# Optimization experiments

Hardware: AMD Instinct MI355X
Metric: run time of the kernel (lower is better)

The kernel has to match this reference:

```python
import jax, jax.numpy as jnp
import numpy as np

# ---- LIF moment-mapping constants (MNN defaults: V_th=20, V_res=0, L=0.05, T_ref=5) ----
L_COND = 0.05
SQRT_L = float(np.sqrt(L_COND))
V_TH, V_RES, T_REF = 20.0, 0.0, 5.0
CLIP = 4.0            # clamp integration bounds to keep exp(x^2) in fp32 range
BN_EPS = 1e-5
SQRT_PI_HALF = float(np.sqrt(np.pi) / 2.0)

_nodes, _weights = np.polynomial.legendre.leggauss(16)
NODES = jnp.asarray(_nodes, jnp.float32)     # [Q]
WEIGHTS = jnp.asarray(_weights, jnp.float32)  # [Q]


def _g(x):
    # Dawson-like integrand: e^{x^2} * sqrt(pi)/2 * (1 + erf(x))
    return jnp.exp(x * x) * (SQRT_PI_HALF * (1.0 + jax.lax.erf(x)))


def _q(t):
    # integrand of the second-order (variance) Dawson function
    e = SQRT_PI_HALF * (1.0 + jax.lax.erf(t))
    return jnp.exp(t * t) * e * e


def _moment_activation(u, s, rho):
    """Mnn_Activate_Mean / Std / Corr: LIF moment mapping via fixed Gauss-Legendre quadrature."""
    s_safe = jnp.maximum(s, 1e-6)
    ub = jnp.clip((V_TH * L_COND - u) / (s_safe * SQRT_L), -CLIP, CLIP)
    lb = jnp.clip((V_RES * L_COND - u) / (s_safe * SQRT_L), -CLIP, CLIP)
    mid, half = 0.5 * (ub + lb), 0.5 * (ub - lb)
    x = mid[..., None] + half[..., None] * NODES            # [B,N,Q]
    I1 = half * jnp.sum(WEIGHTS * _g(x), axis=-1)           # int_{lb}^{ub} g
    u_a = 1.0 / (T_REF + (2.0 / L_COND) * I1)               # mean firing rate
    # variance of ISI: (8/L^2) int_{lb}^{ub} e^{x^2} h(x) dx, h(x)= int_{-CLIP}^{x} q(t) dt
    hm = 0.5 * (x + CLIP)                                   # inner half-width, [B,N,Q]
    t = 0.5 * (x - CLIP)[..., None] + hm[..., None] * NODES  # [B,N,Q,Q]
    h = hm * jnp.sum(WEIGHTS * _q(t), axis=-1)              # [B,N,Q]
    V = half * jnp.sum(WEIGHTS * jnp.exp(x * x) * h, axis=-1)
    var_T = (8.0 / (L_COND * L_COND)) * V
    s_a = jnp.sqrt(jnp.maximum(u_a ** 3 * var_T, 0.0))      # std of firing rate
    # linear-response susceptibility for correlation propagation
    chi = u_a * u_a * (2.0 / L_COND) * (_g(ub) - _g(lb)) / (SQRT_L * jnp.maximum(s_a, 1e-6))
    rho_a = rho * chi[:, :, None] * chi[:, None, :]
    n = rho.shape[-1]
    idx = jnp.arange(n)
    rho_a = rho_a.at[:, idx, idx].set(1.0)
    return u_a, s_a, rho_a


def setup_inputs() -> dict:
    key = jax.random.key(0)
    k = jax.random.split(key, 6)
    B, NIN, NOUT = 512, 256, 256
    u = jax.random.normal(k[0], (B, NIN), jnp.float32) + 1.0
    s = jax.random.uniform(k[1], (B, NIN), jnp.float32, minval=0.1, maxval=1.5)
    # valid correlation matrix: normalized low-rank Gram matrix
    A = jax.random.normal(k[2], (B, NIN, 64), jnp.float32)
    cov = jnp.einsum('bik,bjk->bij', A, A) / 64.0
    d = jnp.sqrt(jnp.diagonal(cov, axis1=1, axis2=2))
    rho = cov / (d[:, :, None] * d[:, None, :] + 1e-6)
    W = jax.random.normal(k[3], (NOUT, NIN), jnp.float32) / np.sqrt(NIN)
    b = jax.random.normal(k[4], (NOUT,), jnp.float32) * 0.01
    gamma = jnp.full((NOUT,), 2.5, jnp.float32)  # bn_mean.weight filled with 2.5
    beta = jnp.full((NOUT,), 2.5, jnp.float32)   # bn_mean.bias filled with 2.5
    return {"u": u, "s": s, "rho": rho, "W": W, "b": b, "gamma": gamma, "beta": beta}


def reference(u, s, rho, W, b, gamma, beta):
    # Mnn_Linear_Corr: propagate (mean, std, corr) through a linear map
    u2 = u @ W.T + b                                        # [B,NOUT]
    cov = rho * s[:, :, None] * s[:, None, :]               # input covariance
    cov = jnp.einsum('oi,bij->boj', W, cov)
    cov = jnp.einsum('boj,pj->bop', cov, W)                 # W C W^T
    var_diag = jnp.diagonal(cov, axis1=1, axis2=2)
    s2 = jnp.sqrt(jnp.maximum(var_diag, 0.0))
    rho2 = cov / (s2[:, :, None] * s2[:, None, :] + 1e-12)
    # BatchNorm1d on mean (training stats) + consistent std scaling (Mnn_Std_Bn1d, bias=False)
    mu = jnp.mean(u2, axis=0)
    var = jnp.mean((u2 - mu) ** 2, axis=0)
    inv = gamma / jnp.sqrt(var + BN_EPS)
    s_bn = s2 * jnp.abs(inv)
    u_bn = (u2 - mu) * inv + beta
    return _moment_activation(u_bn, s_bn, rho2)
```

## Files before the change

kernel.cpp:

```cpp
#include <hip/hip_runtime.h>
#include <math.h>

#define NB 512
#define NN 256

typedef __bf16 bf16x8 __attribute__((ext_vector_type(8)));
typedef float f32x16 __attribute__((ext_vector_type(16)));

constexpr float C_ERF   = 0.88622692545275801f;
constexpr float SQRT_PI = 1.77245385090551603f;
constexpr float SQRTL   = 0.22360679774997896f;

__device__ __constant__ float GLN[16] = {
  -0.98940093499164993f, -0.94457502307323258f, -0.86563120238783174f,
  -0.75540440835500303f, -0.61787624440264375f, -0.45801677765722739f,
  -0.28160355077925891f, -0.09501250983763744f,  0.09501250983763744f,
   0.28160355077925891f,  0.45801677765722739f,  0.61787624440264375f,
   0.75540440835500303f,  0.86563120238783174f,  0.94457502307323258f,
   0.98940093499164993f };
__device__ __constant__ float GLW[16] = {
   0.02715245941175409f, 0.06225352393864789f, 0.09515851168249278f,
   0.12462897125553387f, 0.14959598881657673f, 0.16915651939500254f,
   0.18260341504492358f, 0.18945061045506850f, 0.18945061045506850f,
   0.18260341504492358f, 0.16915651939500254f, 0.14959598881657673f,
   0.12462897125553387f, 0.09515851168249278f, 0.06225352393864789f,
   0.02715245941175409f };

__device__ __forceinline__ float fast_P(float z) {
  float r = __builtin_amdgcn_rcpf(fmaf(0.5f, z, 1.0f));
  float p = fmaf(r, 0.17087277f, -0.82215223f);
  p = fmaf(r, p, 1.48851587f);
  p = fmaf(r, p, -1.13520398f);
  p = fmaf(r, p, 0.27886807f);
  p = fmaf(r, p, -0.18628806f);
  p = fmaf(r, p, 0.09678418f);
  p = fmaf(r, p, 0.37409196f);
  p = fmaf(r, p, 1.00002368f);
  p = fmaf(r, p, -1.26551223f);
  return C_ERF * r * __expf(p);
}
__device__ __forceinline__ float fast_EE(float x, float E) {
  float P = fast_P(fabsf(x));
  return x <= 0.0f ? P : fmaf(SQRT_PI, E, -P);
}

__device__ __forceinline__ uint bfrn(float x) {
  uint u = __float_as_uint(x);
  return (u + 0x7fffu + ((u >> 16) & 1u)) >> 16;
}
__device__ __forceinline__ uint packhi(float a, float b) {
  return bfrn(a) | (bfrn(b) << 16);
}
__device__ __forceinline__ uint packlo(float a, float b, uint h) {
  float af = __uint_as_float(h << 16);
  float bf = __uint_as_float(h & 0xffff0000u);
  return bfrn(a - af) | (bfrn(b - bf) << 16);
}
__device__ __forceinline__ void stage8(ushort* hiP, ushort* loP, int row, int halfk,
                                       float4 f0, float4 f1) {
  uint h0 = packhi(f0.x, f0.y), h1 = packhi(f0.z, f0.w);
  uint h2 = packhi(f1.x, f1.y), h3 = packhi(f1.z, f1.w);
  uint l0 = packlo(f0.x, f0.y, h0), l1 = packlo(f0.z, f0.w, h1);
  uint l2 = packlo(f1.x, f1.y, h2), l3 = packlo(f1.z, f1.w, h3);
  int lane = halfk * 32 + (row & 31);
  int base = ((row >> 5) * 64 + lane) * 8;
  *(uint4*)&hiP[base] = make_uint4(h0, h1, h2, h3);
  *(uint4*)&loP[base] = make_uint4(l0, l1, l2, l3);
}

__global__ __launch_bounds__(256) void k_u2(const float* __restrict__ u,
                                            const float* __restrict__ W,
                                            const float* __restrict__ bias,
                                            float* __restrict__ u2) {
  int b = blockIdx.x, t = threadIdx.x;
  __shared__ __align__(16) float su[NN];
  su[t] = u[b * NN + t];
  __syncthreads();
  const float4* su4 = (const float4*)su;
  const float4* W4  = (const float4*)(W + t * NN);
  float acc = bias[t];
  #pragma unroll 8
  for (int i = 0; i < NN / 4; ++i) {
    float4 wv = W4[i];
    float4 uv = su4[i];
    acc = fmaf(wv.x, uv.x, acc); acc = fmaf(wv.y, uv.y, acc);
    acc = fmaf(wv.z, uv.z, acc); acc = fmaf(wv.w, uv.w, acc);
  }
  u2[b * NN + t] = acc;
}

__global__ __launch_bounds__(256) void k_bn(const float* __restrict__ u2,
                                            const float* __restrict__ gamma,
                                            float* __restrict__ muv,
                                            float* __restrict__ invv) {
  int o = blockIdx.x, t = threadIdx.x;
  float v1 = u2[t * NN + o];
  float v2 = u2[(t + 256) * NN + o];
  __shared__ float rs[256], rq[256];
  rs[t] = v1 + v2;
  rq[t] = v1 * v1 + v2 * v2;
  __syncthreads();
  for (int off = 128; off > 0; off >>= 1) {
    if (t < off) { rs[t] += rs[t + off]; rq[t] += rq[t + off]; }
    __syncthreads();
  }
  if (t == 0) {
    float m   = rs[0] * (1.0f / NB);
    float var = rq[0] * (1.0f / NB) - m * m;
    muv[o]  = m;
    invv[o] = gamma[o] * rsqrtf(var + 1e-5f);
  }
}

__global__ __launch_bounds__(256) void k_gemm1(const float* __restrict__ W,
                                               const float* __restrict__ s,
                                               const float* __restrict__ rho,
                                               float* __restrict__ T, int c0) {
  __shared__ ushort sAh[2048], sAl[2048], sBh[2048], sBl[2048];
  int t = threadIdx.x;
  int m0 = blockIdx.x * 128, n0 = blockIdx.y * 128;
  int bl = blockIdx.z, bg = c0 + bl;
  const float* Rb = rho + (size_t)bg * (NN * NN);
  const float* sb = s + bg * NN;
  int row = t >> 1, halfk = t & 1;
  int w = t >> 6, lane = t & 63;
  int mb0 = (w & 1) * 2, nb0 = (w >> 1) * 2;

  f32x16 acc[2][2] = {};

  const float* Aptr = W + (m0 + row) * NN + halfk * 8;
  const float* Bptr = Rb + (n0 + row) * NN + halfk * 8;
  const float* Sptr = sb + halfk * 8;
  float4 a0 = *(const float4*)(Aptr);
  float4 a1 = *(const float4*)(Aptr + 4);
  float4 b0 = *(const float4*)(Bptr);
  float4 b1 = *(const float4*)(Bptr + 4);
  float4 sv0 = *(const float4*)(Sptr);
  float4 sv1 = *(const float4*)(Sptr + 4);

  for (int kk = 0; kk < NN; kk += 16) {
    float4 as0 = make_float4(a0.x * sv0.x, a0.y * sv0.y, a0.z * sv0.z, a0.w * sv0.w);
    float4 as1 = make_float4(a1.x * sv1.x, a1.y * sv1.y, a1.z * sv1.z, a1.w * sv1.w);
    stage8(sAh, sAl, row, halfk, as0, as1);
    stage8(sBh, sBl, row, halfk, b0, b1);
    __syncthreads();
    if (kk + 16 < NN) {
      a0 = *(const float4*)(Aptr + kk + 16);
      a1 = *(const float4*)(Aptr + kk + 20);
      b0 = *(const float4*)(Bptr + kk + 16);
      b1 = *(const float4*)(Bptr + kk + 20);
      sv0 = *(const float4*)(Sptr + kk + 16);
      sv1 = *(const float4*)(Sptr + kk + 20);
    }
    bf16x8 ah[2], al[2], bh[2], blv[2];
    #pragma unroll
    for (int i = 0; i < 2; ++i) {
      ah[i]  = *(const bf16x8*)&sAh[((mb0 + i) * 64 + lane) * 8];
      al[i]  = *(const bf16x8*)&sAl[((mb0 + i) * 64 + lane) * 8];
      bh[i]  = *(const bf16x8*)&sBh[((nb0 + i) * 64 + lane) * 8];
      blv[i] = *(const bf16x8*)&sBl[((nb0 + i) * 64 + lane) * 8];
    }
    #pragma unroll
    for (int mi = 0; mi < 2; ++mi)
      #pragma unroll
      for (int ni = 0; ni < 2; ++ni) {
        acc[mi][ni] = __builtin_amdgcn_mfma_f32_32x32x16_bf16(ah[mi], bh[ni],  acc[mi][ni], 0, 0, 0);
        acc[mi][ni] = __builtin_amdgcn_mfma_f32_32x32x16_bf16(al[mi], bh[ni],  acc[mi][ni], 0, 0, 0);
        acc[mi][ni] = __builtin_amdgcn_mfma_f32_32x32x16_bf16(ah[mi], blv[ni], acc[mi][ni], 0, 0, 0);
        acc[mi][ni] = __builtin_amdgcn_mfma_f32_32x32x16_bf16(al[mi], blv[ni], acc[mi][ni], 0, 0, 0);
      }
    __syncthreads();
  }

  float* Tb = T + (size_t)bl * (NN * NN);
  int r2 = lane >> 5, col = lane & 31;
  int wm = (w & 1) * 64, wn = (w >> 1) * 64;
  #pragma unroll
  for (int mi = 0; mi < 2; ++mi)
    #pragma unroll
    for (int r = 0; r < 16; ++r) {
      int orow = m0 + wm + mi * 32 + (r & 3) + 8 * (r >> 2) + 4 * r2;
      #pragma unroll
      for (int ni = 0; ni < 2; ++ni) {
        int pcol = n0 + wn + ni * 32 + col;
        Tb[orow * NN + pcol] = acc[mi][ni][r];
      }
    }
}

__global__ __launch_bounds__(256) void k_diag(const float* __restrict__ T,
                                              const float* __restrict__ W,
                                              const float* __restrict__ s,
                                              float* __restrict__ s2v, int c0) {
  int wid = threadIdx.x >> 6, lane = threadIdx.x & 63;
  int idx = blockIdx.x * 4 + wid;
  int bl = idx >> 8, o = idx & 255;
  int bg = c0 + bl;
  const float* Trow = T + (size_t)bl * (NN * NN) + o * NN;
  const float* Wrow = W + o * NN;
  const float* sb = s + bg * NN;
  float4 tv = *(const float4*)(Trow + lane * 4);
  float4 wv = *(const float4*)(Wrow + lane * 4);
  float4 sv = *(const float4*)(sb + lane * 4);
  float p = tv.x * wv.x * sv.x + tv.y * wv.y * sv.y +
            tv.z * wv.z * sv.z + tv.w * wv.w * sv.w;
  for (int off = 32; off; off >>= 1) p += __shfl_down(p, off, 64);
  if (lane == 0) s2v[bg * NN + o] = sqrtf(fmaxf(p, 0.0f));
}

__global__ __launch_bounds__(256) void k_act(const float* __restrict__ u2,
                                             const float* __restrict__ muv,
                                             const float* __restrict__ invv,
                                             const float* __restrict__ beta,
                                             const float* __restrict__ s2v,
                                             float* __restrict__ out_ua,
                                             float* __restrict__ out_sa,
                                             float* __restrict__ chiv, int c0) {
  int t = threadIdx.x;
  int e = blockIdx.x * 128 + (t >> 1);
  int half = t & 1;
  int bg = c0 + (e >> 8);
  int o = e & 255;
  int id = bg * NN + o;
  float iv  = invv[o];
  float ubn = fmaf(u2[id] - muv[o], iv, beta[o]);
  float sbn = s2v[id] * fabsf(iv);

  float ss = fmaxf(sbn, 1e-6f);
  float isl = 1.0f / (ss * SQRTL);
  float ub = fminf(fmaxf((1.0f - ubn) * isl, -4.0f), 4.0f);
  float lb = fminf(fmaxf((0.0f - ubn) * isl, -4.0f), 4.0f);
  float mid = 0.5f * (ub + lb), haf = 0.5f * (ub - lb);

  float I1 = 0.0f, V = 0.0f;
  for (int k = half; k < 16; k += 2) {
    float x  = fmaf(haf, GLN[k], mid);
    float E  = __expf(x * x);
    float EEx = fast_EE(x, E);
    I1 = fmaf(GLW[k], EEx, I1);
    float hm = 0.5f * (x + 4.0f);
    float tb = 0.5f * (x - 4.0f);
    float hs = 0.0f;
    #pragma unroll 4
    for (int j = 0; j < 16; ++j) {
      float tj = fmaf(hm, GLN[j], tb);
      float Et = __expf(tj * tj);
      float EEt = fast_EE(tj, Et);
      hs = fmaf(GLW[j], EEt * EEt * __builtin_amdgcn_rcpf(Et), hs);
    }
    V = fmaf(GLW[k], E * (hm * hs), V);
  }
  I1 += __shfl_xor(I1, 1);
  V  += __shfl_xor(V, 1);
  if (half == 0) {
    I1 *= haf; V *= haf;
    float u_a  = 1.0f / fmaf(40.0f, I1, 5.0f);
    float varT = 3200.0f * V;
    float s_a  = sqrtf(fmaxf(u_a * u_a * u_a * varT, 0.0f));
    float gub = fast_EE(ub, __expf(ub * ub));
    float glb = fast_EE(lb, __expf(lb * lb));
    float chi  = u_a * u_a * 40.0f * (gub - glb) / (SQRTL * fmaxf(s_a, 1e-6f));
    out_ua[id] = u_a;
    out_sa[id] = s_a;
    chiv[id]   = chi;
  }
}

__global__ __launch_bounds__(256) void k_gemm2(const float* __restrict__ T,
                                               const float* __restrict__ W,
                                               const float* __restrict__ s,
                                               const float* __restrict__ s2v,
                                               const float* __restrict__ chiv,
                                               float* __restrict__ out_rho, int c0) {
  __shared__ ushort sAh[2048], sAl[2048], sBh[2048], sBl[2048];
  int t = threadIdx.x;
  int m0 = blockIdx.x * 128, n0 = blockIdx.y * 128;
  int bl = blockIdx.z, bg = c0 + bl;
  const float* Tb = T + (size_t)bl * (NN * NN);
  const float* sb = s + bg * NN;
  int row = t >> 1, halfk = t & 1;
  int w = t >> 6, lane = t & 63;
  int mb0 = (w & 1) * 2, nb0 = (w >> 1) * 2;

  f32x16 acc[2][2] = {};

  const float* Aptr = Tb + (m0 + row) * NN + halfk * 8;
  const float* Bptr = W + (n0 + row) * NN + halfk * 8;
  const float* Sptr = sb + halfk * 8;
  float4 a0 = *(const float4*)(Aptr);
  float4 a1 = *(const float4*)(Aptr + 4);
  float4 b0 = *(const float4*)(Bptr);
  float4 b1 = *(const float4*)(Bptr + 4);
  float4 sv0 = *(const float4*)(Sptr);
  float4 sv1 = *(const float4*)(Sptr + 4);

  for (int kk = 0; kk < NN; kk += 16) {
    float4 bs0 = make_float4(b0.x * sv0.x, b0.y * sv0.y, b0.z * sv0.z, b0.w * sv0.w);
    float4 bs1 = make_float4(b1.x * sv1.x, b1.y * sv1.y, b1.z * sv1.z, b1.w * sv1.w);
    stage8(sAh, sAl, row, halfk, a0, a1);
    stage8(sBh, sBl, row, halfk, bs0, bs1);
    __syncthreads();
    if (kk + 16 < NN) {
      a0 = *(const float4*)(Aptr + kk + 16);
      a1 = *(const float4*)(Aptr + kk + 20);
      b0 = *(const float4*)(Bptr + kk + 16);
      b1 = *(const float4*)(Bptr + kk + 20);
      sv0 = *(const float4*)(Sptr + kk + 16);
      sv1 = *(const float4*)(Sptr + kk + 20);
    }
    bf16x8 ah[2], al[2], bh[2], blv[2];
    #pragma unroll
    for (int i = 0; i < 2; ++i) {
      ah[i]  = *(const bf16x8*)&sAh[((mb0 + i) * 64 + lane) * 8];
      al[i]  = *(const bf16x8*)&sAl[((mb0 + i) * 64 + lane) * 8];
      bh[i]  = *(const bf16x8*)&sBh[((nb0 + i) * 64 + lane) * 8];
      blv[i] = *(const bf16x8*)&sBl[((nb0 + i) * 64 + lane) * 8];
    }
    #pragma unroll
    for (int mi = 0; mi < 2; ++mi)
      #pragma unroll
      for (int ni = 0; ni < 2; ++ni) {
        acc[mi][ni] = __builtin_amdgcn_mfma_f32_32x32x16_bf16(ah[mi], bh[ni],  acc[mi][ni], 0, 0, 0);
        acc[mi][ni] = __builtin_amdgcn_mfma_f32_32x32x16_bf16(al[mi], bh[ni],  acc[mi][ni], 0, 0, 0);
        acc[mi][ni] = __builtin_amdgcn_mfma_f32_32x32x16_bf16(ah[mi], blv[ni], acc[mi][ni], 0, 0, 0);
      }
    __syncthreads();
  }

  float* Ob = out_rho + (size_t)bg * (NN * NN);
  int r2 = lane >> 5, col = lane & 31;
  int wm = (w & 1) * 64, wn = (w >> 1) * 64;
  float chp[2], szp[2];
  #pragma unroll
  for (int ni = 0; ni < 2; ++ni) {
    int p = n0 + wn + ni * 32 + col;
    chp[ni] = chiv[bg * NN + p];
    szp[ni] = s2v[bg * NN + p];
  }
  #pragma unroll
  for (int mi = 0; mi < 2; ++mi)
    #pragma unroll
    for (int r = 0; r < 16; ++r) {
      int orow = m0 + wm + mi * 32 + (r & 3) + 8 * (r >> 2) + 4 * r2;
      float co = chiv[bg * NN + orow];
      float so = s2v[bg * NN + orow];
      #pragma unroll
      for (int ni = 0; ni < 2; ++ni) {
        int pcol = n0 + wn + ni * 32 + col;
        float v = acc[mi][ni][r] * co * chp[ni] *
                  __builtin_amdgcn_rcpf(fmaf(so, szp[ni], 1e-12f));
        if (orow == pcol) v = 1.0f;
        Ob[orow * NN + pcol] = v;
      }
    }
}

extern "C" void kernel_launch(void* const* d_in, const int* in_sizes, int n_in,
                              void* d_out, int out_size, void* d_ws, size_t ws_size,
                              hipStream_t stream) {
  (void)in_sizes; (void)n_in; (void)out_size;
  const float* u     = (const float*)d_in[0];
  const float* s     = (const float*)d_in[1];
  const float* rho   = (const float*)d_in[2];
  const float* W     = (const float*)d_in[3];
  const float* bias  = (const float*)d_in[4];
  const float* gamma = (const float*)d_in[5];
  const float* beta  = (const float*)d_in[6];

  float* out_ua  = (float*)d_out;
  float* out_sa  = out_ua + NB * NN;
  float* out_rho = out_sa + NB * NN;

  float* u2   = (float*)d_ws;
  float* s2v  = u2 + NB * NN;
  float* chiv = s2v + NB * NN;
  float* muv  = chiv + NB * NN;
  float* invv = muv + NN;
  float* T    = invv + NN;
  size_t used = (size_t)((char*)T - (char*)d_ws);
  size_t rem  = ws_size > used ? ws_size - used : 0;
  int chunk = (int)(rem / ((size_t)NN * NN * 4));
  if (chunk > NB) chunk = NB;
  if (chunk < 1) chunk = 1;

  k_u2<<<NB, 256, 0, stream>>>(u, W, bias, u2);
  k_bn<<<NN, 256, 0, stream>>>(u2, gamma, muv, invv);

  for (int c0 = 0; c0 < NB; c0 += chunk) {
    int cb = (NB - c0) < chunk ? (NB - c0) : chunk;
    dim3 gg(2, 2, cb);
    k_gemm1<<<gg, 256, 0, stream>>>(W, s, rho, T, c0);
    k_diag<<<cb * 64, 256, 0, stream>>>(T, W, s, s2v, c0);
    k_act<<<cb * 2, 256, 0, stream>>>(u2, muv, invv, beta, s2v, out_ua, out_sa, chiv, c0);
    k_gemm2<<<gg, 256, 0, stream>>>(T, W, s, s2v, chiv, out_rho, c0);
  }
}
```

Baseline: 446.9 us.

## Fuse covariance GEMMs, diagonal and activation into one per-batch kernel

```diff
diff --git a/kernel.cpp b/kernel.cpp
--- a/kernel.cpp
+++ b/kernel.cpp
@@ -62,8 +62,7 @@
   uint h2 = packhi(f1.x, f1.y), h3 = packhi(f1.z, f1.w);
   uint l0 = packlo(f0.x, f0.y, h0), l1 = packlo(f0.z, f0.w, h1);
   uint l2 = packlo(f1.x, f1.y, h2), l3 = packlo(f1.z, f1.w, h3);
-  int lane = halfk * 32 + (row & 31);
-  int base = ((row >> 5) * 64 + lane) * 8;
+  int base = ((row >> 5) * 64 + halfk * 32 + (row & 31)) * 8;
   *(uint4*)&hiP[base] = make_uint4(h0, h1, h2, h3);
   *(uint4*)&loP[base] = make_uint4(l0, l1, l2, l3);
 }
@@ -112,24 +111,34 @@
   }
 }
 
-__global__ __launch_bounds__(256) void k_gemm1(const float* __restrict__ W,
-                                               const float* __restrict__ s,
-                                               const float* __restrict__ rho,
-                                               float* __restrict__ T, int c0) {
-  __shared__ ushort sAh[2048], sAl[2048], sBh[2048], sBl[2048];
+__global__ __launch_bounds__(512, 2) void k_fused(
+    const float* __restrict__ W, const float* __restrict__ s,
+    const float* __restrict__ rho, const float* __restrict__ u2,
+    const float* __restrict__ muv, const float* __restrict__ invv,
+    const float* __restrict__ beta, float* __restrict__ out_ua,
+    float* __restrict__ out_sa, float* __restrict__ out_rho) {
+  __shared__ __align__(16) char lds[163840];
+  ushort* Th = (ushort*)lds;
+  ushort* Ah = (ushort*)(lds + 131072);
+  ushort* Al = (ushort*)(lds + 139264);
+  ushort* Bh = (ushort*)(lds + 147456);
+  ushort* Bl = (ushort*)(lds + 155648);
+  float* s2L  = (float*)(lds + 131072);
+  float* chiL = (float*)(lds + 132096);
+
   int t = threadIdx.x;
-  int m0 = blockIdx.x * 128, n0 = blockIdx.y * 128;
-  int bl = blockIdx.z, bg = c0 + bl;
+  int bg = blockIdx.x;
   const float* Rb = rho + (size_t)bg * (NN * NN);
   const float* sb = s + bg * NN;
   int row = t >> 1, halfk = t & 1;
   int w = t >> 6, lane = t & 63;
-  int mb0 = (w & 1) * 2, nb0 = (w >> 1) * 2;
-
-  f32x16 acc[2][2] = {};
-
-  const float* Aptr = W + (m0 + row) * NN + halfk * 8;
-  const float* Bptr = Rb + (n0 + row) * NN + halfk * 8;
+  int wmt = (w & 3) * 2, wnt = (w >> 2) * 4;
+  int wm = wmt * 32, wn = wnt * 32;
+
+  f32x16 acc[2][4] = {};
+
+  const float* Aptr = W  + row * NN + halfk * 8;
+  const float* Bptr = Rb + row * NN + halfk * 8;
   const float* Sptr = sb + halfk * 8;
   float4 a0 = *(const float4*)(Aptr);
   float4 a1 = *(const float4*)(Aptr + 4);
@@ -141,8 +150,8 @@
   for (int kk = 0; kk < NN; kk += 16) {
     float4 as0 = make_float4(a0.x * sv0.x, a0.y * sv0.y, a0.z * sv0.z, a0.w * sv0.w);
     float4 as1 = make_float4(a1.x * sv1.x, a1.y * sv1.y, a1.z * sv1.z, a1.w * sv1.w);
-    stage8(sAh, sAl, row, halfk, as0, as1);
-    stage8(sBh, sBl, row, halfk, b0, b1);
+    stage8(Ah, Al, row, halfk, as0, as1);
+    stage8(Bh, Bl, row, halfk, b0, b1);
     __syncthreads();
     if (kk + 16 < NN) {
       a0 = *(const float4*)(Aptr + kk + 16);
@@ -152,205 +161,176 @@
       sv0 = *(const float4*)(Sptr + kk + 16);
       sv1 = *(const float4*)(Sptr + kk + 20);
     }
-    bf16x8 ah[2], al[2], bh[2], blv[2];
+    bf16x8 ahf[2], alf[2], bhf[4], blf[4];
     #pragma unroll
     for (int i = 0; i < 2; ++i) {
-      ah[i]  = *(const bf16x8*)&sAh[((mb0 + i) * 64 + lane) * 8];
-      al[i]  = *(const bf16x8*)&sAl[((mb0 + i) * 64 + lane) * 8];
-      bh[i]  = *(const bf16x8*)&sBh[((nb0 + i) * 64 + lane) * 8];
-      blv[i] = *(const bf16x8*)&sBl[((nb0 + i) * 64 + lane) * 8];
+      ahf[i] = *(const bf16x8*)&Ah[((wmt + i) * 64 + lane) * 8];
+      alf[i] = *(const bf16x8*)&Al[((wmt + i) * 64 + lane) * 8];
+    }
+    #pragma unroll
+    for (int i = 0; i < 4; ++i) {
+      bhf[i] = *(const bf16x8*)&Bh[((wnt + i) * 64 + lane) * 8];
+      blf[i] = *(const bf16x8*)&Bl[((wnt + i) * 64 + lane) * 8];
     }
     #pragma unroll
     for (int mi = 0; mi < 2; ++mi)
       #pragma unroll
-      for (int ni = 0; ni < 2; ++ni) {
-        acc[mi][ni] = __builtin_amdgcn_mfma_f32_32x32x16_bf16(ah[mi], bh[ni],  acc[mi][ni], 0, 0, 0);
-        acc[mi][ni] = __builtin_amdgcn_mfma_f32_32x32x16_bf16(al[mi], bh[ni],  acc[mi][ni], 0, 0, 0);
-        acc[mi][ni] = __builtin_amdgcn_mfma_f32_32x32x16_bf16(ah[mi], blv[ni], acc[mi][ni], 0, 0, 0);
-        acc[mi][ni] = __builtin_amdgcn_mfma_f32_32x32x16_bf16(al[mi], blv[ni], acc[mi][ni], 0, 0, 0);
-      }
-    __syncthreads();
-  }
-
-  float* Tb = T + (size_t)bl * (NN * NN);
-  int r2 = lane >> 5, col = lane & 31;
-  int wm = (w & 1) * 64, wn = (w >> 1) * 64;
+      for (int ni = 0; ni < 4; ++ni) {
+        acc[mi][ni] = __builtin_amdgcn_mfma_f32_32x32x16_bf16(ahf[mi], bhf[ni], acc[mi][ni], 0, 0, 0);
+        acc[mi][ni] = __builtin_amdgcn_mfma_f32_32x32x16_bf16(alf[mi], bhf[ni], acc[mi][ni], 0, 0, 0);
+        acc[mi][ni] = __builtin_amdgcn_mfma_f32_32x32x16_bf16(ahf[mi], blf[ni], acc[mi][ni], 0, 0, 0);
+      }
+    __syncthreads();
+  }
+
+  if (t < NN) s2L[t] = 0.0f;
   #pragma unroll
   for (int mi = 0; mi < 2; ++mi)
     #pragma unroll
-    for (int r = 0; r < 16; ++r) {
-      int orow = m0 + wm + mi * 32 + (r & 3) + 8 * (r >> 2) + 4 * r2;
-      #pragma unroll
-      for (int ni = 0; ni < 2; ++ni) {
-        int pcol = n0 + wn + ni * 32 + col;
-        Tb[orow * NN + pcol] = acc[mi][ni][r];
-      }
-    }
-}
-
-__global__ __launch_bounds__(256) void k_diag(const float* __restrict__ T,
-                                              const float* __restrict__ W,
-                                              const float* __restrict__ s,
-                                              float* __restrict__ s2v, int c0) {
-  int wid = threadIdx.x >> 6, lane = threadIdx.x & 63;
-  int idx = blockIdx.x * 4 + wid;
-  int bl = idx >> 8, o = idx & 255;
-  int bg = c0 + bl;
-  const float* Trow = T + (size_t)bl * (NN * NN) + o * NN;
-  const float* Wrow = W + o * NN;
-  const float* sb = s + bg * NN;
-  float4 tv = *(const float4*)(Trow + lane * 4);
-  float4 wv = *(const float4*)(Wrow + lane * 4);
-  float4 sv = *(const float4*)(sb + lane * 4);
-  float p = tv.x * wv.x * sv.x + tv.y * wv.y * sv.y +
-            tv.z * wv.z * sv.z + tv.w * wv.w * sv.w;
-  for (int off = 32; off; off >>= 1) p += __shfl_down(p, off, 64);
-  if (lane == 0) s2v[bg * NN + o] = sqrtf(fmaxf(p, 0.0f));
-}
-
-__global__ __launch_bounds__(256) void k_act(const float* __restrict__ u2,
-                                             const float* __restrict__ muv,
-                                             const float* __restrict__ invv,
-                                             const float* __restrict__ beta,
-                                             const float* __restrict__ s2v,
-                                             float* __restrict__ out_ua,
-                                             float* __restrict__ out_sa,
-                                             float* __restrict__ chiv, int c0) {
-  int t = threadIdx.x;
-  int e = blockIdx.x * 128 + (t >> 1);
-  int half = t & 1;
-  int bg = c0 + (e >> 8);
-  int o = e & 255;
-  int id = bg * NN + o;
-  float iv  = invv[o];
-  float ubn = fmaf(u2[id] - muv[o], iv, beta[o]);
-  float sbn = s2v[id] * fabsf(iv);
-
-  float ss = fmaxf(sbn, 1e-6f);
-  float isl = 1.0f / (ss * SQRTL);
-  float ub = fminf(fmaxf((1.0f - ubn) * isl, -4.0f), 4.0f);
-  float lb = fminf(fmaxf((0.0f - ubn) * isl, -4.0f), 4.0f);
-  float mid = 0.5f * (ub + lb), haf = 0.5f * (ub - lb);
-
-  float I1 = 0.0f, V = 0.0f;
-  for (int k = half; k < 16; k += 2) {
-    float x  = fmaf(haf, GLN[k], mid);
-    float E  = __expf(x * x);
-    float EEx = fast_EE(x, E);
-    I1 = fmaf(GLW[k], EEx, I1);
-    float hm = 0.5f * (x + 4.0f);
-    float tb = 0.5f * (x - 4.0f);
-    float hs = 0.0f;
-    #pragma unroll 4
-    for (int j = 0; j < 16; ++j) {
-      float tj = fmaf(hm, GLN[j], tb);
-      float Et = __expf(tj * tj);
-      float EEt = fast_EE(tj, Et);
-      hs = fmaf(GLW[j], EEt * EEt * __builtin_amdgcn_rcpf(Et), hs);
-    }
-    V = fmaf(GLW[k], E * (hm * hs), V);
-  }
-  I1 += __shfl_xor(I1, 1);
-  V  += __shfl_xor(V, 1);
-  if (half == 0) {
-    I1 *= haf; V *= haf;
-    float u_a  = 1.0f / fmaf(40.0f, I1, 5.0f);
-    float varT = 3200.0f * V;
-    float s_a  = sqrtf(fmaxf(u_a * u_a * u_a * varT, 0.0f));
-    float gub = fast_EE(ub, __expf(ub * ub));
-    float glb = fast_EE(lb, __expf(lb * lb));
-    float chi  = u_a * u_a * 40.0f * (gub - glb) / (SQRTL * fmaxf(s_a, 1e-6f));
-    out_ua[id] = u_a;
-    out_sa[id] = s_a;
-    chiv[id]   = chi;
-  }
-}
-
-__global__ __launch_bounds__(256) void k_gemm2(const float* __restrict__ T,
-                                               const float* __restrict__ W,
-                                               const float* __restrict__ s,
-                                               const float* __restrict__ s2v,
-                                               const float* __restrict__ chiv,
-                                               float* __restrict__ out_rho, int c0) {
-  __shared__ ushort sAh[2048], sAl[2048], sBh[2048], sBl[2048];
-  int t = threadIdx.x;
-  int m0 = blockIdx.x * 128, n0 = blockIdx.y * 128;
-  int bl = blockIdx.z, bg = c0 + bl;
-  const float* Tb = T + (size_t)bl * (NN * NN);
-  const float* sb = s + bg * NN;
-  int row = t >> 1, halfk = t & 1;
-  int w = t >> 6, lane = t & 63;
-  int mb0 = (w & 1) * 2, nb0 = (w >> 1) * 2;
-
-  f32x16 acc[2][2] = {};
-
-  const float* Aptr = Tb + (m0 + row) * NN + halfk * 8;
-  const float* Bptr = W + (n0 + row) * NN + halfk * 8;
-  const float* Sptr = sb + halfk * 8;
-  float4 a0 = *(const float4*)(Aptr);
-  float4 a1 = *(const float4*)(Aptr + 4);
-  float4 b0 = *(const float4*)(Bptr);
-  float4 b1 = *(const float4*)(Bptr + 4);
-  float4 sv0 = *(const float4*)(Sptr);
-  float4 sv1 = *(const float4*)(Sptr + 4);
+    for (int ni = 0; ni < 4; ++ni)
+      #pragma unroll
+      for (int r = 0; r < 16; ++r) {
+        int o = wm + mi * 32 + (r & 3) + 8 * (r >> 2) + 4 * (lane >> 5);
+        int j = wn + ni * 32 + (lane & 31);
+        Th[o * NN + ((((j >> 3) ^ (o & 31)) << 3) | (j & 7))] = (ushort)bfrn(acc[mi][ni][r]);
+      }
+  __syncthreads();
+
+  {
+    float sjv[4];
+    #pragma unroll
+    for (int ni = 0; ni < 4; ++ni) sjv[ni] = sb[wn + ni * 32 + (lane & 31)];
+    #pragma unroll
+    for (int mi = 0; mi < 2; ++mi)
+      #pragma unroll
+      for (int r = 0; r < 16; ++r) {
+        int o = wm + mi * 32 + (r & 3) + 8 * (r >> 2) + 4 * (lane >> 5);
+        float v = 0.0f;
+        #pragma unroll
+        for (int ni = 0; ni < 4; ++ni) {
+          int j = wn + ni * 32 + (lane & 31);
+          v = fmaf(acc[mi][ni][r], W[o * NN + j] * sjv[ni], v);
+        }
+        #pragma unroll
+        for (int off = 16; off; off >>= 1) v += __shfl_xor(v, off);
+        if ((lane & 31) == 0) atomicAdd(&s2L[o], v);
+      }
+  }
+  __syncthreads();
+
+  {
+    int e = t >> 1, half = t & 1;
+    int id = bg * NN + e;
+    float iv  = invv[e];
+    float ubn = fmaf(u2[id] - muv[e], iv, beta[e]);
+    float s2v = sqrtf(fmaxf(s2L[e], 0.0f));
+    float sbn = s2v * fabsf(iv);
+    float ss  = fmaxf(sbn, 1e-6f);
+    float isl = 1.0f / (ss * SQRTL);
+    float ub = fminf(fmaxf((1.0f - ubn) * isl, -4.0f), 4.0f);
+    float lb = fminf(fmaxf((0.0f - ubn) * isl, -4.0f), 4.0f);
+    float mid = 0.5f * (ub + lb), haf = 0.5f * (ub - lb);
+    float I1 = 0.0f, V = 0.0f;
+    for (int k = half; k < 16; k += 2) {
+      float x  = fmaf(haf, GLN[k], mid);
+      float E  = __expf(x * x);
+      I1 = fmaf(GLW[k], fast_EE(x, E), I1);
+      float hm = 0.5f * (x + 4.0f);
+      float tb = 0.5f * (x - 4.0f);
+      float hs = 0.0f;
+      #pragma unroll 4
+      for (int j = 0; j < 16; ++j) {
+        float tj = fmaf(hm, GLN[j], tb);
+        float Et = __expf(tj * tj);
+        float EEt = fast_EE(tj, Et);
+        hs = fmaf(GLW[j], EEt * EEt * __builtin_amdgcn_rcpf(Et), hs);
+      }
+      V = fmaf(GLW[k], E * (hm * hs), V);
+    }
+    I1 += __shfl_xor(I1, 1);
+    V  += __shfl_xor(V, 1);
+    if (half == 0) {
+      I1 *= haf; V *= haf;
+      float u_a  = 1.0f / fmaf(40.0f, I1, 5.0f);
+      float varT = 3200.0f * V;
+      float s_a  = sqrtf(fmaxf(u_a * u_a * u_a * varT, 0.0f));
+      float gub = fast_EE(ub, __expf(ub * ub));
+      float glb = fast_EE(lb, __expf(lb * lb));
+      float chi = u_a * u_a * 40.0f * (gub - glb) / (SQRTL * fmaxf(s_a, 1e-6f));
+      out_ua[id] = u_a;
+      out_sa[id] = s_a;
+      chiL[e] = chi;
+      s2L[e]  = s2v;
+    }
+  }
+  __syncthreads();
+
+  #pragma unroll
+  for (int mi = 0; mi < 2; ++mi)
+    #pragma unroll
+    for (int ni = 0; ni < 4; ++ni)
+      #pragma unroll
+      for (int r = 0; r < 16; ++r) acc[mi][ni][r] = 0.0f;
+
+  b0 = *(const float4*)(Aptr);
+  b1 = *(const float4*)(Aptr + 4);
+  sv0 = *(const float4*)(Sptr);
+  sv1 = *(const float4*)(Sptr + 4);
 
   for (int kk = 0; kk < NN; kk += 16) {
     float4 bs0 = make_float4(b0.x * sv0.x, b0.y * sv0.y, b0.z * sv0.z, b0.w * sv0.w);
     float4 bs1 = make_float4(b1.x * sv1.x, b1.y * sv1.y, b1.z * sv1.z, b1.w * sv1.w);
-    stage8(sAh, sAl, row, halfk, a0, a1);
-    stage8(sBh, sBl, row, halfk, bs0, bs1);
+    stage8(Bh, Bl, row, halfk, bs0, bs1);
     __syncthreads();
     if (kk + 16 < NN) {
-      a0 = *(const float4*)(Aptr + kk + 16);
-      a1 = *(const float4*)(Aptr + kk + 20);
-      b0 = *(const float4*)(Bptr + kk + 16);
-      b1 = *(const float4*)(Bptr + kk + 20);
+      b0 = *(const float4*)(Aptr + kk + 16);
+      b1 = *(const float4*)(Aptr + kk + 20);
       sv0 = *(const float4*)(Sptr + kk + 16);
       sv1 = *(const float4*)(Sptr + kk + 20);
     }
-    bf16x8 ah[2], al[2], bh[2], blv[2];
+    bf16x8 af[2], bhf[4], blf[4];
     #pragma unroll
     for (int i = 0; i < 2; ++i) {
-      ah[i]  = *(const bf16x8*)&sAh[((mb0 + i) * 64 + lane) * 8];
-      al[i]  = *(const bf16x8*)&sAl[((mb0 + i) * 64 + lane) * 8];
-      bh[i]  = *(const bf16x8*)&sBh[((nb0 + i) * 64 + lane) * 8];
-      blv[i] = *(const bf16x8*)&sBl[((nb0 + i) * 64 + lane) * 8];
+      int ra = wm + i * 32 + (lane & 31);
+      int jb = (kk >> 3) + (lane >> 5);
+      af[i] = *(const bf16x8*)&Th[ra * NN + ((jb ^ (ra & 31)) << 3)];
+    }
+    #pragma unroll
+    for (int i = 0; i < 4; ++i) {
+      bhf[i] = *(const bf16x8*)&Bh[((wnt + i) * 64 + lane) * 8];
+      blf[i] = *(const bf16x8*)&Bl[((wnt + i) * 64 + lane) * 8];
     }
     #pragma unroll
     for (int mi = 0; mi < 2; ++mi)
       #pragma unroll
-      for (int ni = 0; ni < 2; ++ni) {
-        acc[mi][ni] = __builtin_amdgcn_mfma_f32_32x32x16_bf16(ah[mi], bh[ni],  acc[mi][ni], 0, 0, 0);
-        acc[mi][ni] = __builtin_amdgcn_mfma_f32_32x32x16_bf16(al[mi], bh[ni],  acc[mi][ni], 0, 0, 0);
-        acc[mi][ni] = __builtin_amdgcn_mfma_f32_32x32x16_bf16(ah[mi], blv[ni], acc[mi][ni], 0, 0, 0);
-      }
-    __syncthreads();
-  }
-
+      for (int ni = 0; ni < 4; ++ni) {
+        acc[mi][ni] = __builtin_amdgcn_mfma_f32_32x32x16_bf16(af[mi], bhf[ni], acc[mi][ni], 0, 0, 0);
+        acc[mi][ni] = __builtin_amdgcn_mfma_f32_32x32x16_bf16(af[mi], blf[ni], acc[mi][ni], 0, 0, 0);
+      }
+    __syncthreads();
+  }
+
+  float chp[4], szp[4];
+  #pragma unroll
+  for (int ni = 0; ni < 4; ++ni) {
+    int p = wn + ni * 32 + (lane & 31);
+    chp[ni] = chiL[p];
+    szp[ni] = s2L[p];
+  }
   float* Ob = out_rho + (size_t)bg * (NN * NN);
-  int r2 = lane >> 5, col = lane & 31;
-  int wm = (w & 1) * 64, wn = (w >> 1) * 64;
-  float chp[2], szp[2];
-  #pragma unroll
-  for (int ni = 0; ni < 2; ++ni) {
-    int p = n0 + wn + ni * 32 + col;
-    chp[ni] = chiv[bg * NN + p];
-    szp[ni] = s2v[bg * NN + p];
-  }
   #pragma unroll
   for (int mi = 0; mi < 2; ++mi)
     #pragma unroll
     for (int r = 0; r < 16; ++r) {
-      int orow = m0 + wm + mi * 32 + (r & 3) + 8 * (r >> 2) + 4 * r2;
-      float co = chiv[bg * NN + orow];
-      float so = s2v[bg * NN + orow];
-      #pragma unroll
-      for (int ni = 0; ni < 2; ++ni) {
-        int pcol = n0 + wn + ni * 32 + col;
+      int o = wm + mi * 32 + (r & 3) + 8 * (r >> 2) + 4 * (lane >> 5);
+      float co = chiL[o], so = s2L[o];
+      #pragma unroll
+      for (int ni = 0; ni < 4; ++ni) {
+        int p = wn + ni * 32 + (lane & 31);
         float v = acc[mi][ni][r] * co * chp[ni] *
                   __builtin_amdgcn_rcpf(fmaf(so, szp[ni], 1e-12f));
-        if (orow == pcol) v = 1.0f;
-        Ob[orow * NN + pcol] = v;
+        if (o == p) v = 1.0f;
+        Ob[o * NN + p] = v;
       }
     }
 }
@@ -358,7 +338,7 @@
 extern "C" void kernel_launch(void* const* d_in, const int* in_sizes, int n_in,
                               void* d_out, int out_size, void* d_ws, size_t ws_size,
                               hipStream_t stream) {
-  (void)in_sizes; (void)n_in; (void)out_size;
+  (void)in_sizes; (void)n_in; (void)out_size; (void)ws_size;
   const float* u     = (const float*)d_in[0];
   const float* s     = (const float*)d_in[1];
   const float* rho   = (const float*)d_in[2];
@@ -372,26 +352,11 @@
   float* out_rho = out_sa + NB * NN;
 
   float* u2   = (float*)d_ws;
-  float* s2v  = u2 + NB * NN;
-  float* chiv = s2v + NB * NN;
-  float* muv  = chiv + NB * NN;
+  float* muv  = u2 + NB * NN;
   float* invv = muv + NN;
-  float* T    = invv + NN;
-  size_t used = (size_t)((char*)T - (char*)d_ws);
-  size_t rem  = ws_size > used ? ws_size - used : 0;
-  int chunk = (int)(rem / ((size_t)NN * NN * 4));
-  if (chunk > NB) chunk = NB;
-  if (chunk < 1) chunk = 1;
 
   k_u2<<<NB, 256, 0, stream>>>(u, W, bias, u2);
   k_bn<<<NN, 256, 0, stream>>>(u2, gamma, muv, invv);
-
-  for (int c0 = 0; c0 < NB; c0 += chunk) {
-    int cb = (NB - c0) < chunk ? (NB - c0) : chunk;
-    dim3 gg(2, 2, cb);
-    k_gemm1<<<gg, 256, 0, stream>>>(W, s, rho, T, c0);
-    k_diag<<<cb * 64, 256, 0, stream>>>(T, W, s, s2v, c0);
-    k_act<<<cb * 2, 256, 0, stream>>>(u2, muv, invv, beta, s2v, out_ua, out_sa, chiv, c0);
-    k_gemm2<<<gg, 256, 0, stream>>>(T, W, s, s2v, chiv, out_rho, c0);
-  }
-}
+  k_fused<<<NB, 512, 0, stream>>>(W, s, rho, u2, muv, invv, beta,
+                                  out_ua, out_sa, out_rho);
+}
```

Result: faster. 392.0 us (-12.3%).
